# Kernel optimization log

Measured on AMD Instinct MI355X. Metric: run time of the kernel, lower is better.

## Reference

```python
import jax, jax.numpy as jnp
import numpy as np

PS = 7  # window size
HEADS = 8


def setup_inputs() -> dict:
    key = jax.random.key(0)
    ks = jax.random.split(key, 5)
    b, C, H, W = 2, 384, 224, 224
    x = jax.random.normal(ks[0], (b, C, H, W), dtype=jnp.float32)
    # Conv2d(dim, 3*dim, k=1, bias=False) -> weight [3C, C]
    qkv_w = jax.random.normal(ks[1], (3 * C, C), dtype=jnp.float32) * (1.0 / np.sqrt(C))
    # depthwise Conv2d(3*dim, 3*dim, k=3, groups=3*dim) -> weight [3C, 1, 3, 3]
    dw_w = jax.random.normal(ks[2], (3 * C, 1, 3, 3), dtype=jnp.float32) * (1.0 / 3.0)
    # temperature parameter, initialized to ones like the module
    temperature = jnp.ones((HEADS, 1, 1), dtype=jnp.float32)
    # Conv2d(dim, dim, k=1, bias=False) -> weight [C, C]
    proj_w = jax.random.normal(ks[3], (C, C), dtype=jnp.float32) * (1.0 / np.sqrt(C))
    return {"x": x, "qkv_w": qkv_w, "dw_w": dw_w, "temperature": temperature, "proj_w": proj_w}


def _l2norm(t):
    n = jnp.sqrt(jnp.sum(t * t, axis=-1, keepdims=True))
    return t / jnp.maximum(n, 1e-12)  # matches F.normalize semantics


def reference(x, qkv_w, dw_w, temperature, proj_w):
    b, C, H, W = x.shape
    heads, ps = HEADS, PS
    d = C // heads
    nh, nw = H // ps, W // ps

    # 1x1 conv qkv projection (pointwise -> einsum)
    qkv = jnp.einsum('bchw,oc->bohw', x, qkv_w)
    # depthwise 3x3 conv, padding=1
    qkv = jax.lax.conv_general_dilated(
        qkv, dw_w, window_strides=(1, 1), padding='SAME',
        feature_group_count=3 * C, dimension_numbers=('NCHW', 'OIHW', 'NCHW'))
    q, k, v = jnp.split(qkv, 3, axis=1)

    def to_win(t):
        # b (head d) (nh ps) (nw ps) -> b (nh nw) head d (ps ps)
        t = t.reshape(b, heads, d, nh, ps, nw, ps)
        t = t.transpose(0, 3, 5, 1, 2, 4, 6)
        return t.reshape(b, nh * nw, heads, d, ps * ps)

    q, k, v = to_win(q), to_win(k), to_win(v)
    q = _l2norm(q)
    k = _l2norm(k)

    # channel-transposed attention: d x d scores per window
    attn = jnp.einsum('bwhds,bwhes->bwhde', q, k) * temperature
    attn = jax.nn.softmax(attn, axis=-1)
    out = jnp.einsum('bwhde,bwhes->bwhds', attn, v)

    # inverse rearrange: b (nh nw) head d (ps ps) -> b (head d) (nh ps) (nw ps)
    out = out.reshape(b, nh, nw, heads, d, ps, ps)
    out = out.transpose(0, 3, 4, 1, 5, 2, 6).reshape(b, C, H, W)

    return jnp.einsum('bchw,oc->bohw', out, proj_w)
```

## Files before the change

kernel.cpp:

```cpp
#include <hip/hip_runtime.h>


#define NB     2
#define CC     384
#define C3     1152
#define HH     224
#define WW2    224
#define HW     50176
#define NHEADS 8
#define DD     48
#define PSZ    7
#define NWINS  1024
#define SS     49
#define SSP    50
#define WS50   (NWINS*SSP)

typedef unsigned int  u32;
typedef unsigned short u16;
typedef __bf16 bf16x8 __attribute__((ext_vector_type(8)));
typedef float  f32x4  __attribute__((ext_vector_type(4)));

__device__ __forceinline__ u16 f2bf(float f){
  union { float f; u32 u; } v; v.f = f;
  u32 r = v.u + 0x7FFFu + ((v.u >> 16) & 1u);
  return (u16)(r >> 16);
}
__device__ __forceinline__ float bf2f(u16 h){
  union { u32 u; float f; } v; v.u = ((u32)h) << 16;
  return v.f;
}

__device__ __forceinline__ int swz(int row, int col){
  return row*64 + (col ^ ((row & 7) << 3));
}

__global__ void k_cvt(const float* __restrict__ qw, const float* __restrict__ pw,
                      u16* __restrict__ qwb, u16* __restrict__ pwb){
  int i = blockIdx.x * 256 + threadIdx.x;
  if (i < C3*CC) qwb[i] = f2bf(qw[i]);
  if (i < CC*CC) pwb[i] = f2bf(pw[i]);
}

__global__ void k_sentinel(float* __restrict__ out, int n){
  int i = blockIdx.x * 256 + threadIdx.x;
  if (i < n) out[i] = 12345.0f;
}

template<int B_F32, int OUT_F32>
__global__ __launch_bounds__(256) void k_gemm(const u16* __restrict__ A,
    const void* __restrict__ Bsrc, void* __restrict__ Cdst){
  __shared__ __align__(16) u16 As[128*32];
  __shared__ __align__(16) u16 Bs[128*32];
  const int m0 = blockIdx.x * 128, n0 = blockIdx.y * 128, b = blockIdx.z;
  const int M  = gridDim.x * 128;
  const int tid = threadIdx.x, lane = tid & 63, wv = tid >> 6;
  const int wm = (wv & 1) * 64, wn = (wv >> 1) * 64;
  const int lr = lane & 15, lg = lane >> 4;

  f32x4 acc[4][4];
  #pragma unroll
  for (int i=0;i<4;++i)
    #pragma unroll
    for (int j=0;j<4;++j) acc[i][j] = {0.f,0.f,0.f,0.f};

  for (int kk=0; kk<12; ++kk){
    const int k0 = kk*32;
    __syncthreads();
    #pragma unroll
    for (int i=0;i<2;++i){
      int chunk = i*256 + tid;
      int row = chunk >> 2, c4 = chunk & 3;
      const uint4 v = *(const uint4*)(A + (size_t)(m0+row)*CC + k0 + c4*8);
      *(uint4*)(As + chunk*8) = v;
    }
    {
      const int k2 = (tid >> 4) * 2, nl = tid & 15;
      if (B_F32){
        const float* X = (const float*)Bsrc + (size_t)b*CC*HW + (size_t)(k0+k2)*HW + n0;
        #pragma unroll
        for (int j=0;j<8;++j){
          int n = nl + j*16;
          u32 p = (u32)f2bf(X[n]) | ((u32)f2bf(X[n+HW]) << 16);
          *(u32*)(Bs + n*32 + k2) = p;
        }
      } else {
        const u16* X = (const u16*)Bsrc + (size_t)b*CC*HW + (size_t)(k0+k2)*HW + n0;
        #pragma unroll
        for (int j=0;j<8;++j){
          int n = nl + j*16;
          u32 p = (u32)X[n] | ((u32)X[n+HW] << 16);
          *(u32*)(Bs + n*32 + k2) = p;
        }
      }
    }
    __syncthreads();
    bf16x8 af[4], bfr[4];
    #pragma unroll
    for (int i=0;i<4;++i) af[i]  = *(const bf16x8*)(As + (wm + i*16 + lr)*32 + lg*8);
    #pragma unroll
    for (int j=0;j<4;++j) bfr[j] = *(const bf16x8*)(Bs + (wn + j*16 + lr)*32 + lg*8);
    #pragma unroll
    for (int i=0;i<4;++i)
      #pragma unroll
      for (int j=0;j<4;++j)
        acc[i][j] = __builtin_amdgcn_mfma_f32_16x16x32_bf16(af[i], bfr[j], acc[i][j], 0, 0, 0);
  }
  #pragma unroll
  for (int i=0;i<4;++i){
    #pragma unroll
    for (int j=0;j<4;++j){
      const int row = m0 + wm + i*16 + lg*4;
      const int col = n0 + wn + j*16 + lr;
      if (OUT_F32){
        float* Cp = (float*)Cdst + (size_t)b*M*HW;
        #pragma unroll
        for (int r=0;r<4;++r) Cp[(size_t)(row+r)*HW + col] = acc[i][j][r];
      } else {
        u16* Cp = (u16*)Cdst + (size_t)b*M*HW;
        #pragma unroll
        for (int r=0;r<4;++r) Cp[(size_t)(row+r)*HW + col] = f2bf(acc[i][j][r]);
      }
    }
  }
}

#define DW_LD  228
__global__ __launch_bounds__(256) void k_dw(const u16* __restrict__ qkv,
    const float* __restrict__ dww, u16* __restrict__ qkv2){
  const int wy = blockIdx.x, o0 = blockIdx.y*2, b = blockIdx.z;
  const int tid = threadIdx.x;
  __shared__ __align__(16) u16 lin[2][9*DW_LD];
  __shared__ __align__(16) u16 outb[2][32*SSP];

  const int y0 = wy*PSZ - 1;
  #pragma unroll
  for (int ch=0; ch<2; ++ch){
    const u16* src = qkv + (size_t)(b*C3 + o0 + ch) * HW;
    #pragma unroll
    for (int j=0;j<4;++j){
      int i = tid + j*256;
      if (i < 9*112){
        int r = i / 112, c2 = i - r*112;
        int y = y0 + r;
        u32 v = 0u;
        if (y >= 0 && y < HH) v = *(const u32*)(src + (size_t)y*WW2 + c2*2);
        *(u32*)(lin[ch] + r*DW_LD + 2 + c2*2) = v;
      }
    }
  }
  if (tid < 36){ int ch = tid/18, t = tid%18; int r = t>>1;
                 lin[ch][r*DW_LD + ((t&1) ? 226 : 1)] = 0; }
  if (tid >= 192 && tid < 256){ int t = tid-192; outb[t>>5][(t&31)*SSP + 49] = 0; }
  __syncthreads();

  if (tid < 224){
    const int wx = tid / PSZ, pi = tid - wx*PSZ;
    const int xb = wx * PSZ;
    #pragma unroll
    for (int ch=0; ch<2; ++ch){
      float wk[9];
      #pragma unroll
      for (int i=0;i<9;++i) wk[i] = dww[(o0+ch)*9 + i];
      float row0[9], row1[9], row2[9];
      #pragma unroll
      for (int c=0;c<9;++c){
        row0[c] = bf2f(lin[ch][(pi+0)*DW_LD + xb + c + 1]);
        row1[c] = bf2f(lin[ch][(pi+1)*DW_LD + xb + c + 1]);
        row2[c] = bf2f(lin[ch][(pi+2)*DW_LD + xb + c + 1]);
      }
      u16* ob = outb[ch] + wx*SSP + pi*PSZ;
      #pragma unroll
      for (int pj=0;pj<PSZ;++pj){
        float s = 0.f;
        #pragma unroll
        for (int kx=0;kx<3;++kx){
          s += wk[0*3+kx]*row0[pj+kx];
          s += wk[1*3+kx]*row1[pj+kx];
          s += wk[2*3+kx]*row2[pj+kx];
        }
        ob[pj] = f2bf(s);
      }
    }
  }
  __syncthreads();

  #pragma unroll
  for (int j=0;j<2;++j){
    int i = tid + j*256;
    if (i < 400){
      int ch = i / 200, idx = i - ch*200;
      u16* dst = qkv2 + ((size_t)(b*C3 + o0 + ch)*NWINS + (size_t)wy*32)*SSP;
      *(uint4*)(dst + idx*8) = *(const uint4*)(outb[ch] + idx*8);
    }
  }
}

__global__ __launch_bounds__(256) void k_attn(const u16* __restrict__ qkv2,
    const float* __restrict__ temp, u16* __restrict__ aout){
  const int h = blockIdx.x, win = blockIdx.y, b = blockIdx.z;
  const int tid = threadIdx.x, lane = tid & 63, wv = tid >> 6;
  const int lr = lane & 15, lg = lane >> 4;

  __shared__ __align__(16) u16 q_s[48*64], k_s[48*64], v_t[64*64], p_s[48*64];
  __shared__ float invq[48], invk[48];

  for (int i=tid; i<48*32; i+=256){ ((u32*)q_s)[i]=0u; ((u32*)k_s)[i]=0u; ((u32*)p_s)[i]=0u; }
  for (int i=tid; i<64*32; i+=256) ((u32*)v_t)[i]=0u;
  __syncthreads();

  const u16* qsrc = qkv2 + ((size_t)(b*C3 +        h*DD)*NWINS + win)*SSP;
  const u16* ksrc = qkv2 + ((size_t)(b*C3 + CC   + h*DD)*NWINS + win)*SSP;
  const u16* vsrc = qkv2 + ((size_t)(b*C3 + 2*CC + h*DD)*NWINS + win)*SSP;
  for (int i=tid; i<48*25; i+=256){
    int dc = i / 25, c = i - dc*25;
    size_t off = (size_t)dc*WS50 + 2*c;
    u32 vq = *(const u32*)(qsrc + off);
    u32 vk = *(const u32*)(ksrc + off);
    u32 vv = *(const u32*)(vsrc + off);
    int sw = swz(dc, 2*c);
    *(u32*)(q_s + sw) = vq;
    *(u32*)(k_s + sw) = vk;
    v_t[swz(2*c,   dc)] = (u16)(vv & 0xffffu);
    v_t[swz(2*c+1, dc)] = (u16)(vv >> 16);
  }
  __syncthreads();

  if (tid < 192){
    const int row96 = tid >> 1, half = tid & 1;
    const int rr = (row96 < 48) ? row96 : row96 - 48;
    const u16* a = (row96 < 48) ? q_s : k_s;
    const int s0 = half ? 25 : 0, s1 = half ? 49 : 25;
    float sum = 0.f;
    for (int s=s0; s<s1; ++s){ float v = bf2f(a[swz(rr,s)]); sum += v*v; }
    sum += __shfl_xor(sum, 1);
    if (!half){
      float inv = 1.f / fmaxf(sqrtf(sum), 1e-12f);
      if (row96 < 48) invq[rr] = inv * temp[h]; else invk[rr] = inv;
    }
  }
  __syncthreads();

  if (wv < 3){
    const int ti = wv;
    f32x4 c3[3];
    #pragma unroll
    for (int tj=0;tj<3;++tj) c3[tj] = {0.f,0.f,0.f,0.f};
    #pragma unroll
    for (int tj=0;tj<3;++tj){
      #pragma unroll
      for (int ks=0; ks<2; ++ks){
        bf16x8 a  = *(const bf16x8*)(q_s + swz(ti*16+lr, ks*32 + lg*8));
        bf16x8 bb = *(const bf16x8*)(k_s + swz(tj*16+lr, ks*32 + lg*8));
        c3[tj] = __builtin_amdgcn_mfma_f32_16x16x32_bf16(a, bb, c3[tj], 0,0,0);
      }
    }
    const float ik0 = invk[lr], ik1 = invk[16+lr], ik2 = invk[32+lr];
    #pragma unroll
    for (int r=0;r<4;++r){
      const int row = ti*16 + lg*4 + r;
      const float iq = invq[row];
      float l0 = c3[0][r]*iq*ik0, l1 = c3[1][r]*iq*ik1, l2 = c3[2][r]*iq*ik2;
      float m = fmaxf(fmaxf(l0,l1),l2);
      m = fmaxf(m, __shfl_xor(m,1)); m = fmaxf(m, __shfl_xor(m,2));
      m = fmaxf(m, __shfl_xor(m,4)); m = fmaxf(m, __shfl_xor(m,8));
      float e0 = __expf(l0-m), e1 = __expf(l1-m), e2 = __expf(l2-m);
      float s = e0+e1+e2;
      s += __shfl_xor(s,1); s += __shfl_xor(s,2);
      s += __shfl_xor(s,4); s += __shfl_xor(s,8);
      const float is = 1.f / s;
      p_s[swz(row, lr)]    = f2bf(e0*is);
      p_s[swz(row, 16+lr)] = f2bf(e1*is);
      p_s[swz(row, 32+lr)] = f2bf(e2*is);
    }
  }
  __syncthreads();

  const int wy = win >> 5, wx = win & 31;
  for (int t = wv; t < 12; t += 4){
    int ti = t >> 2, tj = t & 3;
    f32x4 c = {0.f,0.f,0.f,0.f};
    #pragma unroll
    for (int ks=0; ks<2; ++ks){
      bf16x8 a  = *(const bf16x8*)(p_s + swz(ti*16+lr, ks*32 + lg*8));
      bf16x8 bb = *(const bf16x8*)(v_t + swz(tj*16+lr, ks*32 + lg*8));
      c = __builtin_amdgcn_mfma_f32_16x16x32_bf16(a, bb, c, 0,0,0);
    }
    int scol = tj*16 + lr;
    if (scol < SS){
      int pi = scol / PSZ, pj = scol - pi*PSZ;
      size_t px = (size_t)(wy*PSZ + pi)*WW2 + wx*PSZ + pj;
      #pragma unroll
      for (int r=0;r<4;++r){
        int d = ti*16 + lg*4 + r;
        aout[(size_t)(b*CC + h*DD + d)*HW + px] = f2bf(c[r]);
      }
    }
  }
}

extern "C" void kernel_launch(void* const* d_in, const int* in_sizes, int n_in,
                              void* d_out, int out_size, void* d_ws, size_t ws_size,
                              hipStream_t stream) {
  const float* x     = (const float*)d_in[0];
  const float* qkvw  = (const float*)d_in[1];
  const float* dww   = (const float*)d_in[2];
  const float* temp  = (const float*)d_in[3];
  const float* projw = (const float*)d_in[4];
  float* out = (float*)d_out;

  const size_t SZ_QKV   = (size_t)NB*C3*HW*2;
  const size_t SZ_QKV2  = (size_t)NB*C3*NWINS*SSP*2;
  const size_t OFF_QKV2 = SZ_QKV;
  const size_t OFF_W1   = OFF_QKV2 + SZ_QKV2;
  const size_t OFF_W2   = OFF_W1 + (size_t)C3*CC*2;
  const size_t NEEDED   = OFF_W2 + (size_t)CC*CC*2;

  if (ws_size < NEEDED){
    k_sentinel<<<(out_size + 255)/256, 256, 0, stream>>>(out, out_size);
    return;
  }
  char* ws = (char*)d_ws;
  u16* qkv  = (u16*)ws;
  u16* qkv2 = (u16*)(ws + OFF_QKV2);
  u16* ao   = (u16*)ws;
  u16* qwb  = (u16*)(ws + OFF_W1);
  u16* pwb  = (u16*)(ws + OFF_W2);

  k_cvt<<<dim3((C3*CC)/256), 256, 0, stream>>>(qkvw, projw, qwb, pwb);
  k_gemm<1,0><<<dim3(9,392,2), 256, 0, stream>>>(qwb, x, qkv);
  k_dw<<<dim3(32, C3/2, NB), 256, 0, stream>>>(qkv, dww, qkv2);
  k_attn<<<dim3(NHEADS, NWINS, NB), 256, 0, stream>>>(qkv2, temp, ao);
  k_gemm<0,1><<<dim3(3,392,2), 256, 0, stream>>>(pwb, ao, out);
}
```

Before: 633.6 us.

## Transpose activations to pixel-major bf16 and load GEMM tiles via global_load_lds

Adds a transpose kernel that converts x from channel-major fp32 into pixel-major bf16, and changes the attention kernel to write its output pixel-major. With both GEMM operands now K-contiguous, tile loads use direct global-to-LDS 16-byte loads in place of strided 2-byte gathers that went through registers. This trades an extra pass over x for fully coalesced GEMM operand loads. It also reuses the qkv2 workspace region for the transposed input.

```diff
diff --git a/kernel.cpp b/kernel.cpp
--- a/kernel.cpp
+++ b/kernel.cpp
@@ -30,6 +30,14 @@
   return v.f;
 }
 
+typedef __attribute__((address_space(3))) u32 as3_u32;
+typedef __attribute__((address_space(1))) const u32 as1_u32;
+__device__ __forceinline__ void gld16(const void* g, void* l){
+  __builtin_amdgcn_global_load_lds((as1_u32*)(unsigned long long)(g),
+                                   (as3_u32*)(u32)(unsigned long long)(l),
+                                   16, 0, 0);
+}
+
 __device__ __forceinline__ int swz(int row, int col){
   return row*64 + (col ^ ((row & 7) << 3));
 }
@@ -46,9 +54,35 @@
   if (i < n) out[i] = 12345.0f;
 }
 
-template<int B_F32, int OUT_F32>
+#define CPAD 386
+__global__ __launch_bounds__(256) void k_trx(const float* __restrict__ x,
+                                             u16* __restrict__ xt){
+  const int pt = blockIdx.x, b = blockIdx.y, tid = threadIdx.x;
+  __shared__ u16 t[64*CPAD];
+  const float* xb = x + (size_t)b*CC*HW + pt*64;
+  #pragma unroll
+  for (int it=0; it<24; ++it){
+    int i = tid + it*256;
+    int c = i >> 4, p4 = (i & 15)*4;
+    float4 v = *(const float4*)(xb + (size_t)c*HW + p4);
+    t[(p4+0)*CPAD + c] = f2bf(v.x);
+    t[(p4+1)*CPAD + c] = f2bf(v.y);
+    t[(p4+2)*CPAD + c] = f2bf(v.z);
+    t[(p4+3)*CPAD + c] = f2bf(v.w);
+  }
+  __syncthreads();
+  u32* dst = (u32*)(xt + ((size_t)b*HW + (size_t)pt*64)*CC);
+  #pragma unroll
+  for (int it=0; it<48; ++it){
+    int j = tid + it*256;
+    int p = j / 192, c2 = j - p*192;
+    dst[j] = *(const u32*)(t + p*CPAD + c2*2);
+  }
+}
+
+template<int OUT_F32>
 __global__ __launch_bounds__(256) void k_gemm(const u16* __restrict__ A,
-    const void* __restrict__ Bsrc, void* __restrict__ Cdst){
+    const u16* __restrict__ B, void* __restrict__ Cdst){
   __shared__ __align__(16) u16 As[128*32];
   __shared__ __align__(16) u16 Bs[128*32];
   const int m0 = blockIdx.x * 128, n0 = blockIdx.y * 128, b = blockIdx.z;
@@ -56,6 +90,7 @@
   const int tid = threadIdx.x, lane = tid & 63, wv = tid >> 6;
   const int wm = (wv & 1) * 64, wn = (wv >> 1) * 64;
   const int lr = lane & 15, lg = lane >> 4;
+  const u16* Bb = B + (size_t)b*HW*CC;
 
   f32x4 acc[4][4];
   #pragma unroll
@@ -70,28 +105,8 @@
     for (int i=0;i<2;++i){
       int chunk = i*256 + tid;
       int row = chunk >> 2, c4 = chunk & 3;
-      const uint4 v = *(const uint4*)(A + (size_t)(m0+row)*CC + k0 + c4*8);
-      *(uint4*)(As + chunk*8) = v;
-    }
-    {
-      const int k2 = (tid >> 4) * 2, nl = tid & 15;
-      if (B_F32){
-        const float* X = (const float*)Bsrc + (size_t)b*CC*HW + (size_t)(k0+k2)*HW + n0;
-        #pragma unroll
-        for (int j=0;j<8;++j){
-          int n = nl + j*16;
-          u32 p = (u32)f2bf(X[n]) | ((u32)f2bf(X[n+HW]) << 16);
-          *(u32*)(Bs + n*32 + k2) = p;
-        }
-      } else {
-        const u16* X = (const u16*)Bsrc + (size_t)b*CC*HW + (size_t)(k0+k2)*HW + n0;
-        #pragma unroll
-        for (int j=0;j<8;++j){
-          int n = nl + j*16;
-          u32 p = (u32)X[n] | ((u32)X[n+HW] << 16);
-          *(u32*)(Bs + n*32 + k2) = p;
-        }
-      }
+      gld16(A  + (size_t)(m0+row)*CC + k0 + c4*8, As + chunk*8);
+      gld16(Bb + (size_t)(n0+row)*CC + k0 + c4*8, Bs + chunk*8);
     }
     __syncthreads();
     bf16x8 af[4], bfr[4];
@@ -276,6 +291,7 @@
   __syncthreads();
 
   const int wy = win >> 5, wx = win & 31;
+  u16* ab = aout + (size_t)b*HW*CC + (size_t)h*DD;
   for (int t = wv; t < 12; t += 4){
     int ti = t >> 2, tj = t & 3;
     f32x4 c = {0.f,0.f,0.f,0.f};
@@ -288,12 +304,11 @@
     int scol = tj*16 + lr;
     if (scol < SS){
       int pi = scol / PSZ, pj = scol - pi*PSZ;
-      size_t px = (size_t)(wy*PSZ + pi)*WW2 + wx*PSZ + pj;
-      #pragma unroll
-      for (int r=0;r<4;++r){
-        int d = ti*16 + lg*4 + r;
-        aout[(size_t)(b*CC + h*DD + d)*HW + px] = f2bf(c[r]);
-      }
+      size_t p = (size_t)(wy*PSZ + pi)*WW2 + wx*PSZ + pj;
+      u32 lo = (u32)f2bf(c[0]) | ((u32)f2bf(c[1]) << 16);
+      u32 hi = (u32)f2bf(c[2]) | ((u32)f2bf(c[3]) << 16);
+      u32* dst = (u32*)(ab + p*CC + ti*16 + lg*4);
+      dst[0] = lo; dst[1] = hi;
     }
   }
 }
@@ -322,13 +337,15 @@
   char* ws = (char*)d_ws;
   u16* qkv  = (u16*)ws;
   u16* qkv2 = (u16*)(ws + OFF_QKV2);
+  u16* xt   = (u16*)(ws + OFF_QKV2);
   u16* ao   = (u16*)ws;
   u16* qwb  = (u16*)(ws + OFF_W1);
   u16* pwb  = (u16*)(ws + OFF_W2);
 
   k_cvt<<<dim3((C3*CC)/256), 256, 0, stream>>>(qkvw, projw, qwb, pwb);
-  k_gemm<1,0><<<dim3(9,392,2), 256, 0, stream>>>(qwb, x, qkv);
+  k_trx<<<dim3(784, NB), 256, 0, stream>>>(x, xt);
+  k_gemm<0><<<dim3(9,392,2), 256, 0, stream>>>(qwb, xt, qkv);
   k_dw<<<dim3(32, C3/2, NB), 256, 0, stream>>>(qkv, dww, qkv2);
   k_attn<<<dim3(NHEADS, NWINS, NB), 256, 0, stream>>>(qkv2, temp, ao);
-  k_gemm<0,1><<<dim3(3,392,2), 256, 0, stream>>>(pwb, ao, out);
-}
+  k_gemm<1><<<dim3(3,392,2), 256, 0, stream>>>(pwb, ao, out);
+}
```

Result: faster. 577.4 us (-8.9%).
